# Kernel tuning notes

Hardware: AMD Instinct MI355X
Metric: run time of the kernel (lower is better)

Reference implementation:

```python
import jax, jax.numpy as jnp
import numpy as np

EPS = 1e-6


def setup_inputs() -> dict:
    key = jax.random.key(0)
    ks = jax.random.split(key, 7)
    b, n, d, H, hid = 4, 512, 128, 4, 32
    scale1 = 1.0 / np.sqrt(2 * d)
    scale2 = 1.0 / np.sqrt(hid)
    return {
        "x": jax.random.normal(ks[0], (b, n, d), dtype=jnp.float32),
        "W1": jax.random.normal(ks[1], (H, 2 * d, hid), dtype=jnp.float32) * scale1,
        "b1": jax.random.normal(ks[2], (H, hid), dtype=jnp.float32) * scale1,
        "W2": jax.random.normal(ks[3], (H, hid), dtype=jnp.float32) * scale2,
        "b2": jax.random.normal(ks[4], (H,), dtype=jnp.float32) * scale2,
        "Wp": jax.random.normal(ks[5], (d, d), dtype=jnp.float32) / np.sqrt(d),
        "bp": jax.random.normal(ks[6], (d,), dtype=jnp.float32) / np.sqrt(d),
    }


def reference(x, W1, b1, W2, b2, Wp, bp):
    # x: [b, n, d]; W1: [H, 2d, hid]; W2: [H, hid]
    d = x.shape[-1]
    # squared pairwise distance via gram matrix: ||xi - xj||^2
    sq = jnp.sum(x * x, axis=-1)                                   # [b, n]
    gram = jnp.einsum("bnd,bmd->bnm", x, x)                        # [b, n, n]
    dist2 = jnp.maximum(sq[:, :, None] + sq[:, None, :] - 2.0 * gram, 0.0)
    # per-head first linear on cat([xi, xj]) split into two projections
    ai = jnp.einsum("bnd,hdk->bhnk", x, W1[:, :d, :])              # [b, H, n, hid]
    aj = jnp.einsum("bnd,hdk->bhnk", x, W1[:, d:, :])              # [b, H, n, hid]
    pre = jnp.tanh(ai[:, :, :, None, :] + aj[:, :, None, :, :]
                   + b1[None, :, None, None, :])                   # [b, H, n, n, hid]
    sigma = jax.nn.softplus(jnp.einsum("bhnmk,hk->bhnm", pre, W2)
                            + b2[None, :, None, None])             # [b, H, n, n]
    adj = jnp.exp(-dist2[:, None, :, :] / (2.0 * sigma * sigma + EPS))
    adj_mean = jnp.mean(adj, axis=1)                               # [b, n, n]
    h = jnp.einsum("bnm,bmd->bnd", adj_mean, x)                    # [b, n, d]
    return h @ Wp + bp
```

## Files before the change

kernel.cpp:

```cpp
#include <hip/hip_runtime.h>

typedef float v4f __attribute__((ext_vector_type(4)));
typedef float v2f __attribute__((ext_vector_type(2)));

#define LOG2E   1.4426950408889634f
#define NLOG2E (-1.4426950408889634f)
#define C2L2E   2.8853900817779268f
#define NM2L2E (-2.8853900817779268f)
#define LN2     0.6931471805599453f

__device__ __forceinline__ float fexp2(float x){ return __builtin_amdgcn_exp2f(x); }
__device__ __forceinline__ float flog2(float x){ return __builtin_amdgcn_logf(x); }
__device__ __forceinline__ float frcp (float x){ return __builtin_amdgcn_rcpf(x); }
__device__ __forceinline__ float hsum(v4f v){ return (v.x+v.y)+(v.z+v.w); }

__global__ __launch_bounds__(256) void prep_kernel(
    const float* __restrict__ x, const float* __restrict__ W1,
    const float* __restrict__ b1, const float* __restrict__ Wp,
    float* __restrict__ sq, float* __restrict__ Abuf,
    float* __restrict__ Bbuf, float* __restrict__ xpT)
{
  const int bid = blockIdx.x, t = threadIdx.x;
  if (bid >= 192) {
    int row = (bid - 192) * 256 + t;
    const v4f* xv = (const v4f*)(x + row * 128);
    float s = 0.f;
#pragma unroll
    for (int q = 0; q < 32; q++) { v4f v = xv[q]; s += hsum(v * v); }
    sq[row] = s;
    return;
  }
  __shared__ v4f Xs[64 * 9];
  __shared__ v4f Ws[32 * 16];
  const bool isAB = bid < 128;
  int it, ct;
  if (isAB) { it = bid >> 2; ct = bid & 3; }
  else      { int q = bid - 128; it = q >> 1; ct = q & 1; }
  const int row0 = it * 64;
  const int tx = t & 15, ty = t >> 4;
  const int r0 = ty * 4, c0 = tx * 4;
  v4f acc[4] = {};

  for (int dd0 = 0; dd0 < 128; dd0 += 32) {
    __syncthreads();
#pragma unroll
    for (int s2 = 0; s2 < 2; s2++) {
      int idx = t + s2 * 256;
      int row = idx >> 3, k4 = idx & 7;
      v4f v = *(const v4f*)(x + (row0 + row) * 128 + dd0 + k4 * 4);
      Xs[row * 9 + ((k4 + (row >> 2)) & 7)] = v;
    }
#pragma unroll
    for (int s2 = 0; s2 < 2; s2++) {
      int idx = t + s2 * 256;
      int dd = idx >> 4, cf4 = idx & 15;
      v4f v;
      if (isAB) {
        int cl = cf4 * 4; int half = cl >> 5; int k = cl & 31;
        v = *(const v4f*)(W1 + (ct * 256 + half * 128 + dd0 + dd) * 32 + k);
      } else {
        v = *(const v4f*)(Wp + (dd0 + dd) * 128 + ct * 64 + cf4 * 4);
      }
      Ws[dd * 16 + cf4] = v;
    }
    __syncthreads();
#pragma unroll
    for (int dd4 = 0; dd4 < 8; dd4++) {
      int sa = (dd4 + ty) & 7;
      v4f a0 = Xs[(r0 + 0) * 9 + sa], a1 = Xs[(r0 + 1) * 9 + sa];
      v4f a2 = Xs[(r0 + 2) * 9 + sa], a3 = Xs[(r0 + 3) * 9 + sa];
#pragma unroll
      for (int u = 0; u < 4; u++) {
        v4f bv = Ws[(dd4 * 4 + u) * 16 + tx];
        acc[0] += a0[u] * bv; acc[1] += a1[u] * bv;
        acc[2] += a2[u] * bv; acc[3] += a3[u] * bv;
      }
    }
  }

  if (isAB) {
    const int h = ct; const int half = c0 >> 5; const int k = c0 & 31;
    v4f bias = {};
    if (half == 0) bias = *(const v4f*)(b1 + h * 32 + k);
    float* dst = (half == 0) ? Abuf : Bbuf;
#pragma unroll
    for (int i = 0; i < 4; i++) {
      int rg = row0 + r0 + i; int b = rg >> 9; int ir = rg & 511;
      v4f o = (acc[i] + bias) * C2L2E;
      v4f eo = { fexp2(o.x), fexp2(o.y), fexp2(o.z), fexp2(o.w) };
      *(v4f*)(dst + ((b * 4 + h) * 512 + ir) * 32 + k) = eo;
    }
  } else {
    int rg0 = row0 + r0; int b = rg0 >> 9; int ir0 = rg0 & 511;
#pragma unroll
    for (int u = 0; u < 4; u++) {
      int c = ct * 64 + c0 + u;
      v4f o = { acc[0][u], acc[1][u], acc[2][u], acc[3][u] };
      *(v4f*)(xpT + (b * 128 + c) * 512 + ir0) = o;
    }
  }
}

__global__ __launch_bounds__(256) void adj_kernel(
    const float* __restrict__ x, const float* __restrict__ sq,
    const float* __restrict__ Abuf, const float* __restrict__ Bbuf,
    const float* __restrict__ W2, const float* __restrict__ b2g,
    float* __restrict__ ADJ)
{
  const int jt = blockIdx.x;
  const int it = blockIdx.y;
  const int b  = blockIdx.z;
  const int t = threadIdx.x, tx = t & 15, ty = t >> 4;
  const int c0 = 2 * tx;
  __shared__ v4f Bs[2 * 32 * 9];
  __shared__ v4f W2s[32];
  __shared__ v2f W2p[32];
  __shared__ float hb[4];

  if (t < 32) {
    v4f w = ((const v4f*)W2)[t] * NM2L2E;
    W2s[t] = w;
    v2f p = { w.x + w.y, w.z + w.w };
    W2p[t] = p;
  }
  if (t < 4) {
    float s = b2g[t];
    for (int k = 0; k < 32; k++) s += W2[t * 32 + k];
    hb[t] = s * LOG2E;
  }

  const int s_col = (t >> 3) & 31, s_k4 = t & 7;
  const int s_slot = (s_k4 + (s_col >> 1)) & 7;

  const float* xb = x + (size_t)b * 512 * 128;
  const int irow = it * 16 + ty;
  const float* xi  = xb + irow * 128;
  const float* xjc = xb + (jt * 32) * 128;

  v4f gacc0 = {}, gacc1 = {};
  for (int half = 0; half < 2; half++) {
    if (half) __syncthreads();
#pragma unroll
    for (int s = 0; s < 2; s++) {
      Bs[s * 288 + s_col * 9 + s_slot] =
        *(const v4f*)(xjc + s_col * 128 + half * 64 + s * 32 + s_k4 * 4);
    }
    __syncthreads();
#pragma unroll
    for (int sec = 0; sec < 2; sec++) {
#pragma unroll
      for (int k4 = 0; k4 < 8; k4++) {
        v4f a0 = *(const v4f*)(xi + half * 64 + sec * 32 + k4 * 4);
        int sb = (k4 + tx) & 7;
        v4f b0  = Bs[sec * 288 + (c0 + 0) * 9 + sb];
        v4f b1v = Bs[sec * 288 + (c0 + 1) * 9 + sb];
        gacc0 += a0 * b0; gacc1 += a0 * b1v;
      }
    }
  }
  float si  = sq[b * 512 + irow];
  float sj0 = sq[b * 512 + jt * 32 + c0], sj1 = sq[b * 512 + jt * 32 + c0 + 1];
  float d2L0 = fmaxf(si + sj0 - 2.f * hsum(gacc0), 0.f) * NLOG2E;
  float d2L1 = fmaxf(si + sj1 - 2.f * hsum(gacc1), 0.f) * NLOG2E;

  float accA0 = 0.f, accA1 = 0.f;
  for (int g = 0; g < 2; g++) {
    __syncthreads();
#pragma unroll
    for (int s = 0; s < 2; s++) {
      Bs[s * 288 + s_col * 9 + s_slot] =
        *(const v4f*)(Bbuf + ((size_t)((b * 4 + g * 2 + s) * 512 + jt * 32 + s_col)) * 32 + s_k4 * 4);
    }
    __syncthreads();
#pragma unroll
    for (int hh = 0; hh < 2; hh++) {
      int h = g * 2 + hh;
      const float* A0 = Abuf + ((size_t)((b * 4 + h) * 512 + irow)) * 32;
      float hbv = hb[h];
      float s0 = hbv, s1 = hbv;
#pragma unroll
      for (int k4 = 0; k4 < 8; k4++) {
        v4f a0 = *(const v4f*)(A0 + k4 * 4);
        int sb = (k4 + tx) & 7;
        v4f bv0 = Bs[hh * 288 + (c0 + 0) * 9 + sb];
        v4f bv1 = Bs[hh * 288 + (c0 + 1) * 9 + sb];
        v4f w  = W2s[h * 8 + k4];
        v2f wp = W2p[h * 8 + k4];
        {
          v4f e = a0 * bv0;
          float d01 = fmaf(e.x, e.y, e.x + e.y) + 1.f;
          float d23 = fmaf(e.z, e.w, e.z + e.w) + 1.f;
          float n01 = fmaf(w.x, e.y, wp.x); n01 = fmaf(w.y, e.x, n01);
          float n23 = fmaf(w.z, e.w, wp.y); n23 = fmaf(w.w, e.z, n23);
          float num = fmaf(n01, d23, n23 * d01);
          s0 = fmaf(num, frcp(d01 * d23), s0);
        }
        {
          v4f e = a0 * bv1;
          float d01 = fmaf(e.x, e.y, e.x + e.y) + 1.f;
          float d23 = fmaf(e.z, e.w, e.z + e.w) + 1.f;
          float n01 = fmaf(w.x, e.y, wp.x); n01 = fmaf(w.y, e.x, n01);
          float n23 = fmaf(w.z, e.w, wp.y); n23 = fmaf(w.w, e.z, n23);
          float num = fmaf(n01, d23, n23 * d01);
          s1 = fmaf(num, frcp(d01 * d23), s1);
        }
      }
      float u20 = fexp2(s0), u21 = fexp2(s1);
      float sg0 = LN2 * flog2(1.f + u20);
      float sg1 = LN2 * flog2(1.f + u21);
      float den0 = fmaf(2.f * sg0, sg0, 1e-6f);
      float den1 = fmaf(2.f * sg1, sg1, 1e-6f);
      float rr = frcp(den0 * den1);
      accA0 += fexp2(d2L0 * (rr * den1));
      accA1 += fexp2(d2L1 * (rr * den0));
    }
  }
  v2f o = { accA0 * 0.25f, accA1 * 0.25f };
  *(v2f*)(ADJ + ((size_t)(b * 512 + irow)) * 512 + jt * 32 + c0) = o;
}

__global__ __launch_bounds__(256) void out_kernel(
    const float* __restrict__ ADJ, const float* __restrict__ xpT,
    const float* __restrict__ bp, float* __restrict__ out)
{
  const int ct = blockIdx.x;
  const int it = blockIdx.y;
  const int b = blockIdx.z;
  const int t = threadIdx.x, tx = t & 15, ty = t >> 4;
  const int r0 = 2 * ty, c0 = 2 * tx;
  __shared__ v4f Ajs[32 * 9], Xps[32 * 9];
  v4f acc[4] = {};
  const int row = t >> 3, k4l = t & 7, slot = (k4l + (row >> 1)) & 7;

  for (int k0 = 0; k0 < 512; k0 += 32) {
    __syncthreads();
    Ajs[row * 9 + slot] = *(const v4f*)(ADJ + ((size_t)(b * 512 + it * 32 + row)) * 512 + k0 + k4l * 4);
    Xps[row * 9 + slot] = *(const v4f*)(xpT + ((size_t)(b * 128 + ct * 32 + row)) * 512 + k0 + k4l * 4);
    __syncthreads();
#pragma unroll
    for (int k4 = 0; k4 < 8; k4++) {
      int sa = (k4 + ty) & 7, sb = (k4 + tx) & 7;
      v4f a0 = Ajs[(r0 + 0) * 9 + sa], a1 = Ajs[(r0 + 1) * 9 + sa];
      v4f b0 = Xps[(c0 + 0) * 9 + sb], b1v = Xps[(c0 + 1) * 9 + sb];
      acc[0] += a0 * b0; acc[1] += a0 * b1v;
      acc[2] += a1 * b0; acc[3] += a1 * b1v;
    }
  }
  float bp0 = bp[ct * 32 + c0], bp1 = bp[ct * 32 + c0 + 1];
  float* dst = out + ((size_t)(b * 512 + it * 32 + r0)) * 128 + ct * 32 + c0;
  v2f o0 = { hsum(acc[0]) + bp0, hsum(acc[1]) + bp1 };
  v2f o1 = { hsum(acc[2]) + bp0, hsum(acc[3]) + bp1 };
  *(v2f*)dst = o0;
  *(v2f*)(dst + 128) = o1;
}

extern "C" void kernel_launch(void* const* d_in, const int* in_sizes, int n_in,
                              void* d_out, int out_size, void* d_ws, size_t ws_size,
                              hipStream_t stream) {
  const float* x  = (const float*)d_in[0];
  const float* W1 = (const float*)d_in[1];
  const float* b1 = (const float*)d_in[2];
  const float* W2 = (const float*)d_in[3];
  const float* b2 = (const float*)d_in[4];
  const float* Wp = (const float*)d_in[5];
  const float* bp = (const float*)d_in[6];
  float* out = (float*)d_out;

  float* ws  = (float*)d_ws;
  float* sq  = ws;
  float* A   = ws + 2048;
  float* Bb  = A + 262144;
  float* xpT = Bb + 262144;
  float* ADJ = xpT + 262144;

  prep_kernel<<<200, 256, 0, stream>>>(x, W1, b1, Wp, sq, A, Bb, xpT);
  adj_kernel<<<dim3(16, 32, 4), 256, 0, stream>>>(x, sq, A, Bb, W2, b2, ADJ);
  out_kernel<<<dim3(4, 16, 4), 256, 0, stream>>>(ADJ, xpT, bp, out);
}
```

Baseline: 61.70 us.

## Store EB in k4-major layout and read directly from global instead of LDS staging

The prep kernel now writes the B-side exponentials in a [b,h,k4,n,4] layout so that consecutive columns are contiguous per k-quad. The adj kernel then loads the B operands straight from global/L2 with vector loads rather than staging them through shared memory. This removes two __syncthreads per head pair and the LDS staging traffic. The cost is more global/cache loads per thread, since each B value is now fetched by every row thread rather than shared through LDS.

```diff
diff --git a/kernel.cpp b/kernel.cpp
--- a/kernel.cpp
+++ b/kernel.cpp
@@ -17,8 +17,8 @@
 __global__ __launch_bounds__(256) void prep_kernel(
     const float* __restrict__ x, const float* __restrict__ W1,
     const float* __restrict__ b1, const float* __restrict__ Wp,
-    float* __restrict__ sq, float* __restrict__ Abuf,
-    float* __restrict__ Bbuf, float* __restrict__ xpT)
+    float* __restrict__ sq, float* __restrict__ EA,
+    float* __restrict__ EB, float* __restrict__ xpT)
 {
   const int bid = blockIdx.x, t = threadIdx.x;
   if (bid >= 192) {
@@ -82,13 +82,16 @@
     const int h = ct; const int half = c0 >> 5; const int k = c0 & 31;
     v4f bias = {};
     if (half == 0) bias = *(const v4f*)(b1 + h * 32 + k);
-    float* dst = (half == 0) ? Abuf : Bbuf;
 #pragma unroll
     for (int i = 0; i < 4; i++) {
       int rg = row0 + r0 + i; int b = rg >> 9; int ir = rg & 511;
       v4f o = (acc[i] + bias) * C2L2E;
       v4f eo = { fexp2(o.x), fexp2(o.y), fexp2(o.z), fexp2(o.w) };
-      *(v4f*)(dst + ((b * 4 + h) * 512 + ir) * 32 + k) = eo;
+      if (half == 0) {
+        *(v4f*)(EA + ((size_t)((b * 4 + h) * 512 + ir)) * 32 + k) = eo;
+      } else {
+        *(v4f*)(EB + ((size_t)(b * 4 + h) * 8 + (k >> 2)) * 2048 + ir * 4) = eo;
+      }
     }
   } else {
     int rg0 = row0 + r0; int b = rg0 >> 9; int ir0 = rg0 & 511;
@@ -103,7 +106,7 @@
 
 __global__ __launch_bounds__(256) void adj_kernel(
     const float* __restrict__ x, const float* __restrict__ sq,
-    const float* __restrict__ Abuf, const float* __restrict__ Bbuf,
+    const float* __restrict__ EA, const float* __restrict__ EB,
     const float* __restrict__ W2, const float* __restrict__ b2g,
     float* __restrict__ ADJ)
 {
@@ -164,56 +167,46 @@
   float d2L1 = fmaxf(si + sj1 - 2.f * hsum(gacc1), 0.f) * NLOG2E;
 
   float accA0 = 0.f, accA1 = 0.f;
-  for (int g = 0; g < 2; g++) {
-    __syncthreads();
-#pragma unroll
-    for (int s = 0; s < 2; s++) {
-      Bs[s * 288 + s_col * 9 + s_slot] =
-        *(const v4f*)(Bbuf + ((size_t)((b * 4 + g * 2 + s) * 512 + jt * 32 + s_col)) * 32 + s_k4 * 4);
-    }
-    __syncthreads();
-#pragma unroll
-    for (int hh = 0; hh < 2; hh++) {
-      int h = g * 2 + hh;
-      const float* A0 = Abuf + ((size_t)((b * 4 + h) * 512 + irow)) * 32;
-      float hbv = hb[h];
-      float s0 = hbv, s1 = hbv;
-#pragma unroll
-      for (int k4 = 0; k4 < 8; k4++) {
-        v4f a0 = *(const v4f*)(A0 + k4 * 4);
-        int sb = (k4 + tx) & 7;
-        v4f bv0 = Bs[hh * 288 + (c0 + 0) * 9 + sb];
-        v4f bv1 = Bs[hh * 288 + (c0 + 1) * 9 + sb];
-        v4f w  = W2s[h * 8 + k4];
-        v2f wp = W2p[h * 8 + k4];
-        {
-          v4f e = a0 * bv0;
-          float d01 = fmaf(e.x, e.y, e.x + e.y) + 1.f;
-          float d23 = fmaf(e.z, e.w, e.z + e.w) + 1.f;
-          float n01 = fmaf(w.x, e.y, wp.x); n01 = fmaf(w.y, e.x, n01);
-          float n23 = fmaf(w.z, e.w, wp.y); n23 = fmaf(w.w, e.z, n23);
-          float num = fmaf(n01, d23, n23 * d01);
-          s0 = fmaf(num, frcp(d01 * d23), s0);
-        }
-        {
-          v4f e = a0 * bv1;
-          float d01 = fmaf(e.x, e.y, e.x + e.y) + 1.f;
-          float d23 = fmaf(e.z, e.w, e.z + e.w) + 1.f;
-          float n01 = fmaf(w.x, e.y, wp.x); n01 = fmaf(w.y, e.x, n01);
-          float n23 = fmaf(w.z, e.w, wp.y); n23 = fmaf(w.w, e.z, n23);
-          float num = fmaf(n01, d23, n23 * d01);
-          s1 = fmaf(num, frcp(d01 * d23), s1);
-        }
-      }
-      float u20 = fexp2(s0), u21 = fexp2(s1);
-      float sg0 = LN2 * flog2(1.f + u20);
-      float sg1 = LN2 * flog2(1.f + u21);
-      float den0 = fmaf(2.f * sg0, sg0, 1e-6f);
-      float den1 = fmaf(2.f * sg1, sg1, 1e-6f);
-      float rr = frcp(den0 * den1);
-      accA0 += fexp2(d2L0 * (rr * den1));
-      accA1 += fexp2(d2L1 * (rr * den0));
-    }
+#pragma unroll 1
+  for (int h = 0; h < 4; h++) {
+    const float* A0 = EA + ((size_t)((b * 4 + h) * 512 + irow)) * 32;
+    const float* Bk = EB + (size_t)(b * 4 + h) * 16384 + (jt * 32 + c0) * 4;
+    float hbv = hb[h];
+    float s0 = hbv, s1 = hbv;
+#pragma unroll
+    for (int k4 = 0; k4 < 8; k4++) {
+      v4f a0 = *(const v4f*)(A0 + k4 * 4);
+      v4f eb0 = *(const v4f*)(Bk + k4 * 2048);
+      v4f eb1 = *(const v4f*)(Bk + k4 * 2048 + 4);
+      v4f w  = W2s[h * 8 + k4];
+      v2f wp = W2p[h * 8 + k4];
+      {
+        v4f e = a0 * eb0;
+        float d01 = fmaf(e.x, e.y, e.x + e.y) + 1.f;
+        float d23 = fmaf(e.z, e.w, e.z + e.w) + 1.f;
+        float n01 = fmaf(w.x, e.y, wp.x); n01 = fmaf(w.y, e.x, n01);
+        float n23 = fmaf(w.z, e.w, wp.y); n23 = fmaf(w.w, e.z, n23);
+        float num = fmaf(n01, d23, n23 * d01);
+        s0 = fmaf(num, frcp(d01 * d23), s0);
+      }
+      {
+        v4f e = a0 * eb1;
+        float d01 = fmaf(e.x, e.y, e.x + e.y) + 1.f;
+        float d23 = fmaf(e.z, e.w, e.z + e.w) + 1.f;
+        float n01 = fmaf(w.x, e.y, wp.x); n01 = fmaf(w.y, e.x, n01);
+        float n23 = fmaf(w.z, e.w, wp.y); n23 = fmaf(w.w, e.z, n23);
+        float num = fmaf(n01, d23, n23 * d01);
+        s1 = fmaf(num, frcp(d01 * d23), s1);
+      }
+    }
+    float u20 = fexp2(s0), u21 = fexp2(s1);
+    float sg0 = LN2 * flog2(1.f + u20);
+    float sg1 = LN2 * flog2(1.f + u21);
+    float den0 = fmaf(2.f * sg0, sg0, 1e-6f);
+    float den1 = fmaf(2.f * sg1, sg1, 1e-6f);
+    float rr = frcp(den0 * den1);
+    accA0 += fexp2(d2L0 * (rr * den1));
+    accA1 += fexp2(d2L1 * (rr * den0));
   }
   v2f o = { accA0 * 0.25f, accA1 * 0.25f };
   *(v2f*)(ADJ + ((size_t)(b * 512 + irow)) * 512 + jt * 32 + c0) = o;
@@ -268,12 +261,12 @@
 
   float* ws  = (float*)d_ws;
   float* sq  = ws;
-  float* A   = ws + 2048;
-  float* Bb  = A + 262144;
-  float* xpT = Bb + 262144;
+  float* EA  = ws + 2048;
+  float* EB  = EA + 262144;
+  float* xpT = EB + 262144;
   float* ADJ = xpT + 262144;
 
-  prep_kernel<<<200, 256, 0, stream>>>(x, W1, b1, Wp, sq, A, Bb, xpT);
-  adj_kernel<<<dim3(16, 32, 4), 256, 0, stream>>>(x, sq, A, Bb, W2, b2, ADJ);
+  prep_kernel<<<200, 256, 0, stream>>>(x, W1, b1, Wp, sq, EA, EB, xpT);
+  adj_kernel<<<dim3(16, 32, 4), 256, 0, stream>>>(x, sq, EA, EB, W2, b2, ADJ);
   out_kernel<<<dim3(4, 16, 4), 256, 0, stream>>>(ADJ, xpT, bp, out);
 }
```

Result: slower. 71.55 us (+16.0%).

## Split-K the output GEMM and halve prep tiles to raise block counts

Applied to the files above, without the earlier changes.

The prep kernel now uses 32-row tiles instead of 64-row tiles, doubling its block count from 200 to 392. The output GEMM is split four ways along K, giving 1024 blocks that write partial sums. A new reduce kernel adds the partials and the bias. The aim is to fill more compute units on the small prep and output stages, at the cost of an extra launch and extra partial-sum traffic through global memory.

```diff
diff --git a/kernel.cpp b/kernel.cpp
--- a/kernel.cpp
+++ b/kernel.cpp
@@ -17,12 +17,12 @@
 __global__ __launch_bounds__(256) void prep_kernel(
     const float* __restrict__ x, const float* __restrict__ W1,
     const float* __restrict__ b1, const float* __restrict__ Wp,
-    float* __restrict__ sq, float* __restrict__ Abuf,
-    float* __restrict__ Bbuf, float* __restrict__ xpT)
+    float* __restrict__ sq, float* __restrict__ EA,
+    float* __restrict__ EB, float* __restrict__ xpT)
 {
   const int bid = blockIdx.x, t = threadIdx.x;
-  if (bid >= 192) {
-    int row = (bid - 192) * 256 + t;
+  if (bid >= 384) {
+    int row = (bid - 384) * 256 + t;
     const v4f* xv = (const v4f*)(x + row * 128);
     float s = 0.f;
 #pragma unroll
@@ -30,26 +30,24 @@
     sq[row] = s;
     return;
   }
-  __shared__ v4f Xs[64 * 9];
+  __shared__ v4f Xs[32 * 9];
   __shared__ v4f Ws[32 * 16];
-  const bool isAB = bid < 128;
+  const bool isAB = bid < 256;
   int it, ct;
   if (isAB) { it = bid >> 2; ct = bid & 3; }
-  else      { int q = bid - 128; it = q >> 1; ct = q & 1; }
-  const int row0 = it * 64;
+  else      { int q = bid - 256; it = q >> 1; ct = q & 1; }
+  const int row0 = it * 32;
   const int tx = t & 15, ty = t >> 4;
-  const int r0 = ty * 4, c0 = tx * 4;
-  v4f acc[4] = {};
+  const int r0 = ty * 2, c0 = tx * 4;
+  v4f acc[2] = {};
+
+  const int s_row = t >> 3, s_k4 = t & 7;
+  const int s_slot = (s_k4 + (s_row >> 1)) & 7;
 
   for (int dd0 = 0; dd0 < 128; dd0 += 32) {
     __syncthreads();
-#pragma unroll
-    for (int s2 = 0; s2 < 2; s2++) {
-      int idx = t + s2 * 256;
-      int row = idx >> 3, k4 = idx & 7;
-      v4f v = *(const v4f*)(x + (row0 + row) * 128 + dd0 + k4 * 4);
-      Xs[row * 9 + ((k4 + (row >> 2)) & 7)] = v;
-    }
+    Xs[s_row * 9 + s_slot] =
+      *(const v4f*)(x + (row0 + s_row) * 128 + dd0 + s_k4 * 4);
 #pragma unroll
     for (int s2 = 0; s2 < 2; s2++) {
       int idx = t + s2 * 256;
@@ -68,12 +66,10 @@
     for (int dd4 = 0; dd4 < 8; dd4++) {
       int sa = (dd4 + ty) & 7;
       v4f a0 = Xs[(r0 + 0) * 9 + sa], a1 = Xs[(r0 + 1) * 9 + sa];
-      v4f a2 = Xs[(r0 + 2) * 9 + sa], a3 = Xs[(r0 + 3) * 9 + sa];
 #pragma unroll
       for (int u = 0; u < 4; u++) {
         v4f bv = Ws[(dd4 * 4 + u) * 16 + tx];
         acc[0] += a0[u] * bv; acc[1] += a1[u] * bv;
-        acc[2] += a2[u] * bv; acc[3] += a3[u] * bv;
       }
     }
   }
@@ -82,21 +78,21 @@
     const int h = ct; const int half = c0 >> 5; const int k = c0 & 31;
     v4f bias = {};
     if (half == 0) bias = *(const v4f*)(b1 + h * 32 + k);
-    float* dst = (half == 0) ? Abuf : Bbuf;
-#pragma unroll
-    for (int i = 0; i < 4; i++) {
+    float* dst = (half == 0) ? EA : EB;
+#pragma unroll
+    for (int i = 0; i < 2; i++) {
       int rg = row0 + r0 + i; int b = rg >> 9; int ir = rg & 511;
       v4f o = (acc[i] + bias) * C2L2E;
       v4f eo = { fexp2(o.x), fexp2(o.y), fexp2(o.z), fexp2(o.w) };
-      *(v4f*)(dst + ((b * 4 + h) * 512 + ir) * 32 + k) = eo;
+      *(v4f*)(dst + ((size_t)((b * 4 + h) * 512 + ir)) * 32 + k) = eo;
     }
   } else {
     int rg0 = row0 + r0; int b = rg0 >> 9; int ir0 = rg0 & 511;
 #pragma unroll
     for (int u = 0; u < 4; u++) {
       int c = ct * 64 + c0 + u;
-      v4f o = { acc[0][u], acc[1][u], acc[2][u], acc[3][u] };
-      *(v4f*)(xpT + (b * 128 + c) * 512 + ir0) = o;
+      v2f o = { acc[0][u], acc[1][u] };
+      *(v2f*)(xpT + ((size_t)(b * 128 + c)) * 512 + ir0) = o;
     }
   }
 }
@@ -219,20 +215,20 @@
   *(v2f*)(ADJ + ((size_t)(b * 512 + irow)) * 512 + jt * 32 + c0) = o;
 }
 
-__global__ __launch_bounds__(256) void out_kernel(
+__global__ __launch_bounds__(256) void out_gemm(
     const float* __restrict__ ADJ, const float* __restrict__ xpT,
-    const float* __restrict__ bp, float* __restrict__ out)
+    float* __restrict__ part)
 {
   const int ct = blockIdx.x;
   const int it = blockIdx.y;
-  const int b = blockIdx.z;
+  const int z = blockIdx.z; const int b = z >> 2, ks = z & 3;
   const int t = threadIdx.x, tx = t & 15, ty = t >> 4;
   const int r0 = 2 * ty, c0 = 2 * tx;
   __shared__ v4f Ajs[32 * 9], Xps[32 * 9];
   v4f acc[4] = {};
   const int row = t >> 3, k4l = t & 7, slot = (k4l + (row >> 1)) & 7;
 
-  for (int k0 = 0; k0 < 512; k0 += 32) {
+  for (int k0 = ks * 128; k0 < ks * 128 + 128; k0 += 32) {
     __syncthreads();
     Ajs[row * 9 + slot] = *(const v4f*)(ADJ + ((size_t)(b * 512 + it * 32 + row)) * 512 + k0 + k4l * 4);
     Xps[row * 9 + slot] = *(const v4f*)(xpT + ((size_t)(b * 128 + ct * 32 + row)) * 512 + k0 + k4l * 4);
@@ -246,12 +242,22 @@
       acc[2] += a1 * b0; acc[3] += a1 * b1v;
     }
   }
-  float bp0 = bp[ct * 32 + c0], bp1 = bp[ct * 32 + c0 + 1];
-  float* dst = out + ((size_t)(b * 512 + it * 32 + r0)) * 128 + ct * 32 + c0;
-  v2f o0 = { hsum(acc[0]) + bp0, hsum(acc[1]) + bp1 };
-  v2f o1 = { hsum(acc[2]) + bp0, hsum(acc[3]) + bp1 };
+  float* dst = part + ((size_t)((ks * 4 + b) * 512 + it * 32 + r0)) * 128 + ct * 32 + c0;
+  v2f o0 = { hsum(acc[0]), hsum(acc[1]) };
+  v2f o1 = { hsum(acc[2]), hsum(acc[3]) };
   *(v2f*)dst = o0;
   *(v2f*)(dst + 128) = o1;
+}
+
+__global__ __launch_bounds__(256) void reduce_out(
+    const float* __restrict__ part, const float* __restrict__ bp,
+    float* __restrict__ out)
+{
+  int g = blockIdx.x * 256 + threadIdx.x;
+  const v4f* p = (const v4f*)part;
+  v4f s = (p[g] + p[g + 65536]) + (p[g + 131072] + p[g + 196608]);
+  v4f bv = ((const v4f*)bp)[g & 31];
+  ((v4f*)out)[g] = s + bv;
 }
 
 extern "C" void kernel_launch(void* const* d_in, const int* in_sizes, int n_in,
@@ -268,12 +274,14 @@
 
   float* ws  = (float*)d_ws;
   float* sq  = ws;
-  float* A   = ws + 2048;
-  float* Bb  = A + 262144;
-  float* xpT = Bb + 262144;
+  float* EA  = ws + 2048;
+  float* EB  = EA + 262144;
+  float* xpT = EB + 262144;
   float* ADJ = xpT + 262144;
-
-  prep_kernel<<<200, 256, 0, stream>>>(x, W1, b1, Wp, sq, A, Bb, xpT);
-  adj_kernel<<<dim3(16, 32, 4), 256, 0, stream>>>(x, sq, A, Bb, W2, b2, ADJ);
-  out_kernel<<<dim3(4, 16, 4), 256, 0, stream>>>(ADJ, xpT, bp, out);
-}
+  float* part = ADJ + 1048576;
+
+  prep_kernel<<<392, 256, 0, stream>>>(x, W1, b1, Wp, sq, EA, EB, xpT);
+  adj_kernel<<<dim3(16, 32, 4), 256, 0, stream>>>(x, sq, EA, EB, W2, b2, ADJ);
+  out_gemm<<<dim3(4, 16, 16), 256, 0, stream>>>(ADJ, xpT, part);
+  reduce_out<<<256, 256, 0, stream>>>(part, bp, out);
+}
```

Measured after the change: 79.12 us. +28.2%, slower.
